# Performance work log

Measured on AMD Instinct MI355X. Metric: run time of the kernel, lower is better.

The kernel has to match this reference:

```python
import jax, jax.numpy as jnp
import numpy as np

N = 16384          # points
DIM = 256          # feature dim
HEADS = 8
HD = DIM // HEADS  # head dim = 32
K = 20             # neighbors
MLP_HID = int(DIM * 4.0)
CHUNK = 2048       # query chunk for kNN (avoids N^2 matrix)
EPS = 1e-5
SCALE = HD ** -0.5


def layernorm(x, w, b):
    m = jnp.mean(x, axis=-1, keepdims=True)
    v = jnp.var(x, axis=-1, keepdims=True)
    return (x - m) * jax.lax.rsqrt(v + EPS) * w + b


def knn_graph(positions):
    """Brute-force kNN (squared L2) computed in query chunks. [N, K] indices, self excluded."""
    def chunk_fn(q):  # q: [CHUNK, 3]
        d = jnp.sum((q[:, None, :] - positions[None, :, :]) ** 2, axis=-1)  # [CHUNK, N]
        _, idx = jax.lax.top_k(-d, K + 1)  # ascending distance; first col is self (dist 0)
        return idx[:, 1:]
    idx = jax.lax.map(chunk_fn, positions.reshape(-1, CHUNK, 3))
    return idx.reshape(-1, K)


def setup_inputs() -> dict:
    key = jax.random.key(0)
    ks = jax.random.split(key, 10)
    w = lambda k, s: jax.random.normal(k, s, jnp.float32) * 0.02
    return {
        "x": jax.random.normal(ks[0], (N, DIM), jnp.float32),
        "positions": jax.random.normal(ks[1], (N, 3), jnp.float32),
        "ln1_w": jnp.ones((DIM,), jnp.float32), "ln1_b": jnp.zeros((DIM,), jnp.float32),
        "Wq": w(ks[2], (DIM, DIM)), "bq": jnp.zeros((DIM,), jnp.float32),
        "Wk": w(ks[3], (DIM, DIM)), "bk": jnp.zeros((DIM,), jnp.float32),
        "Wv": w(ks[4], (DIM, DIM)), "bv": jnp.zeros((DIM,), jnp.float32),
        "Wo": w(ks[5], (DIM, DIM)), "bo": jnp.zeros((DIM,), jnp.float32),
        "ln2_w": jnp.ones((DIM,), jnp.float32), "ln2_b": jnp.zeros((DIM,), jnp.float32),
        "W1": w(ks[6], (MLP_HID, DIM)), "b1": jnp.zeros((MLP_HID,), jnp.float32),
        "W2": w(ks[7], (DIM, MLP_HID)), "b2": jnp.zeros((DIM,), jnp.float32),
    }


def reference(x, positions, ln1_w, ln1_b, Wq, bq, Wk, bk, Wv, bv, Wo, bo,
              ln2_w, ln2_b, W1, b1, W2, b2):
    knn = knn_graph(positions)                      # [N, K] int32
    h = layernorm(x, ln1_w, ln1_b)                  # [N, D]
    q = (h @ Wq.T + bq).reshape(N, HEADS, HD)       # [N, H, hd]
    k = h @ Wk.T + bk                               # [N, D]
    v = h @ Wv.T + bv
    kn = k[knn].reshape(N, K, HEADS, HD)            # gather neighbor keys   [N, K, H, hd]
    vn = v[knn].reshape(N, K, HEADS, HD)            # gather neighbor values
    scores = jnp.einsum('nhd,nkhd->nhk', q, kn) * SCALE  # [N, H, K]
    attn = jax.nn.softmax(scores, axis=-1)
    out = jnp.einsum('nhk,nkhd->nhd', attn, vn).reshape(N, DIM)
    x = x + out @ Wo.T + bo                          # residual 1
    h2 = layernorm(x, ln2_w, ln2_b)
    mlp = jax.nn.gelu(h2 @ W1.T + b1, approximate=False) @ W2.T + b2
    return x + mlp                                   # residual 2
```

## Files before the change

kernel.cpp:

```cpp
#include <hip/hip_runtime.h>
#include <math.h>

#define N_PTS 16384
#define DIMS 256
#define HEADS 8
#define HDIM 32
#define KNN 20
#define MLPH 1024
#define NSHARD 128
#define SHARDC 128
#define SURV_SLOTS 64
#define SCALE 0.17677669529663687f

typedef unsigned short u16;
typedef unsigned long long ull;
typedef __attribute__((ext_vector_type(8))) short bf16x8;
typedef __attribute__((ext_vector_type(8))) unsigned short u16x8;
typedef __attribute__((ext_vector_type(4))) float f32x4;

__device__ __forceinline__ float bf2f(u16 u) {
  return __uint_as_float(((unsigned int)u) << 16);
}
__device__ __forceinline__ u16 f2bf(float f) {
  unsigned int u = __float_as_uint(f);
  u += 0x7fffu + ((u >> 16) & 1u);
  return (u16)(u >> 16);
}
__device__ __forceinline__ float fin(float v) {
  return __builtin_isfinite(v) ? v : 0.f;
}
__device__ __forceinline__ float dist2(float4 a, float4 b) {
  float dx = a.x - b.x, dy = a.y - b.y, dz = a.z - b.z;
  return dx * dx + dy * dy + dz * dz;
}
__device__ __forceinline__ u16x8 cvt8(float4 a, float4 b) {
  u16x8 o;
  o[0] = f2bf(a.x); o[1] = f2bf(a.y); o[2] = f2bf(a.z); o[3] = f2bf(a.w);
  o[4] = f2bf(b.x); o[5] = f2bf(b.y); o[6] = f2bf(b.z); o[7] = f2bf(b.w);
  return o;
}
__device__ __forceinline__ void gld16(const u16* g, u16* l) {
  __builtin_amdgcn_global_load_lds(
      (const __attribute__((address_space(1))) unsigned int*)g,
      (__attribute__((address_space(3))) unsigned int*)l, 16, 0, 0);
}


__global__ __launch_bounds__(256) void knn_init(const float* __restrict__ pos,
                                                float4* __restrict__ pos4,
                                                int* __restrict__ cnt,
                                                int* __restrict__ nbr) {
  int i = blockIdx.x * 256 + threadIdx.x;
  cnt[i] = 0;
#pragma unroll
  for (int j = 0; j < KNN; ++j) nbr[i * KNN + j] = 0;
  float x = fin(pos[3 * i]), y = fin(pos[3 * i + 1]), z = fin(pos[3 * i + 2]);
  pos4[i] = make_float4(x, y, z, x * x + y * y + z * z);
}


__global__ __launch_bounds__(256) void conv_w(const float* __restrict__ Wq,
                                              const float* __restrict__ Wk,
                                              const float* __restrict__ Wv,
                                              const float* __restrict__ Wo,
                                              u16* __restrict__ wbf) {
  int idx = blockIdx.x * 256 + threadIdx.x;
  int mat = idx >> 14, loc = idx & 16383;
  const float* src = (mat == 0) ? Wq : ((mat == 1) ? Wk : ((mat == 2) ? Wv : Wo));
  float4 v = ((const float4*)src)[loc];
  ushort4 o;
  o.x = f2bf(v.x); o.y = f2bf(v.y); o.z = f2bf(v.z); o.w = f2bf(v.w);
  ((ushort4*)(wbf + mat * 65536))[loc] = o;
}


__global__ __launch_bounds__(256) void knn_shardmin(const float4* __restrict__ pos4,
                                                    float* __restrict__ Mmin) {
  __shared__ float4 cp[SHARDC];
  int shard = blockIdx.x;
  int qbase = blockIdx.y * 1024 + threadIdx.x;
  if (threadIdx.x < SHARDC) cp[threadIdx.x] = pos4[shard * SHARDC + threadIdx.x];
  float m2x[4], m2y[4], m2z[4], mn[4];
#pragma unroll
  for (int k = 0; k < 4; ++k) {
    float4 qp = pos4[qbase + k * 256];
    m2x[k] = -2.f * qp.x; m2y[k] = -2.f * qp.y; m2z[k] = -2.f * qp.z;
    mn[k] = 3.4e38f;
  }
  __syncthreads();
#pragma unroll 4
  for (int c = 0; c < SHARDC; ++c) {
    float4 cc = cp[c];
#pragma unroll
    for (int k = 0; k < 4; ++k) {
      float t = fmaf(m2z[k], cc.z, cc.w);
      t = fmaf(m2y[k], cc.y, t);
      t = fmaf(m2x[k], cc.x, t);
      mn[k] = fminf(mn[k], t);
    }
  }
#pragma unroll
  for (int k = 0; k < 4; ++k) Mmin[shard * N_PTS + qbase + k * 256] = mn[k];
}

__global__ __launch_bounds__(256) void knn_tau(const float* __restrict__ Mmin,
                                               float* __restrict__ tau) {
  int q = blockIdx.x * 256 + threadIdx.x;
  float a[21];
#pragma unroll
  for (int j = 0; j < 21; ++j) a[j] = 3.4e38f;
  for (int s = 0; s < NSHARD; ++s) {
    float v = Mmin[s * N_PTS + q];
    a[20] = fminf(a[20], v);
#pragma unroll
    for (int j = 20; j >= 1; --j) {
      float lo = fminf(a[j - 1], a[j]), hi = fmaxf(a[j - 1], a[j]);
      a[j - 1] = lo; a[j] = hi;
    }
  }
  tau[q] = a[20];
}

__global__ __launch_bounds__(256) void knn_collect(const float4* __restrict__ pos4,
                                                   const float* __restrict__ tau,
                                                   int* __restrict__ cnt,
                                                   ull* __restrict__ surv) {
  __shared__ float4 cp[SHARDC];
  int cbase = blockIdx.x * SHARDC;
  int qbase = blockIdx.y * 1024 + threadIdx.x;
  if (threadIdx.x < SHARDC) cp[threadIdx.x] = pos4[cbase + threadIdx.x];
  float4 qp[4];
  float m2x[4], m2y[4], m2z[4], tq[4];
  unsigned int packed[4];
  int hitcnt[4];
#pragma unroll
  for (int k = 0; k < 4; ++k) {
    qp[k] = pos4[qbase + k * 256];
    m2x[k] = -2.f * qp[k].x; m2y[k] = -2.f * qp[k].y; m2z[k] = -2.f * qp[k].z;
    tq[k] = tau[qbase + k * 256] + 2e-4f;
    packed[k] = 0; hitcnt[k] = 0;
  }
  __syncthreads();
#pragma unroll 4
  for (int c = 0; c < SHARDC; ++c) {
    float4 cc = cp[c];
#pragma unroll
    for (int k = 0; k < 4; ++k) {
      float t = fmaf(m2z[k], cc.z, cc.w);
      t = fmaf(m2y[k], cc.y, t);
      t = fmaf(m2x[k], cc.x, t);
      bool hit = (t <= tq[k]);
      packed[k] = hit ? ((packed[k] << 8) | (unsigned)c) : packed[k];
      hitcnt[k] += hit ? 1 : 0;
    }
  }
#pragma unroll
  for (int k = 0; k < 4; ++k) {
    int hc = hitcnt[k];
    if (hc > 0) {
      int q = qbase + k * 256;
      if (hc <= 4) {
        int slot = atomicAdd(&cnt[q], hc);
        for (int i = 0; i < hc; ++i) {
          int c = (packed[k] >> (8 * i)) & 255;
          float d = dist2(qp[k], cp[c]);
          ull key = ((ull)__float_as_uint(d) << 32) | (unsigned)(cbase + c);
          if (slot + i < SURV_SLOTS)
            surv[(size_t)q * SURV_SLOTS + slot + i] = key;
        }
      } else {
        for (int c = 0; c < SHARDC; ++c) {
          float4 cc = cp[c];
          float t = fmaf(m2z[k], cc.z, cc.w);
          t = fmaf(m2y[k], cc.y, t);
          t = fmaf(m2x[k], cc.x, t);
          if (t <= tq[k]) {
            float d = dist2(qp[k], cc);
            ull key = ((ull)__float_as_uint(d) << 32) | (unsigned)(cbase + c);
            int slot = atomicAdd(&cnt[q], 1);
            if (slot < SURV_SLOTS) surv[(size_t)q * SURV_SLOTS + slot] = key;
          }
        }
      }
    }
  }
}

__global__ void knn_rank(const int* __restrict__ cnt,
                         const ull* __restrict__ surv,
                         int* __restrict__ nbr) {
  __shared__ ull s[SURV_SLOTS];
  int q = blockIdx.x;
  int c = min(cnt[q], SURV_SLOTS);
  for (int i = threadIdx.x; i < c; i += 64) s[i] = surv[(size_t)q * SURV_SLOTS + i];
  __syncthreads();
  for (int i = threadIdx.x; i < c; i += 64) {
    ull key = s[i];
    int rank = 0;
    for (int j = 0; j < c; ++j) rank += (s[j] < key);
    if (rank >= 1 && rank <= KNN) nbr[q * KNN + rank - 1] = (int)(key & 0xffffffffu);
  }
}


__global__ __launch_bounds__(256) void ln_kernel(const float* __restrict__ xin,
                                                 const float* __restrict__ w,
                                                 const float* __restrict__ b,
                                                 u16* __restrict__ out) {
  int row = blockIdx.x * 4 + (threadIdx.x >> 6);
  int lane = threadIdx.x & 63;
  float4 u = ((const float4*)(xin + row * DIMS))[lane];
  float f[4] = {fin(u.x), fin(u.y), fin(u.z), fin(u.w)};
  float sum = f[0] + f[1] + f[2] + f[3];
  float sq = f[0] * f[0] + f[1] * f[1] + f[2] * f[2] + f[3] * f[3];
#pragma unroll
  for (int o = 32; o > 0; o >>= 1) {
    sum += __shfl_xor(sum, o);
    sq += __shfl_xor(sq, o);
  }
  float mean = sum * (1.f / 256.f);
  float var = fmaxf(sq * (1.f / 256.f) - mean * mean, 0.f);
  float rs = rsqrtf(var + 1e-5f);
  float4 wv = ((const float4*)w)[lane];
  float4 bv = ((const float4*)b)[lane];
  ushort4 o4;
  o4.x = f2bf(fin((f[0] - mean) * rs * wv.x + bv.x));
  o4.y = f2bf(fin((f[1] - mean) * rs * wv.y + bv.y));
  o4.z = f2bf(fin((f[2] - mean) * rs * wv.z + bv.z));
  o4.w = f2bf(fin((f[3] - mean) * rs * wv.w + bv.w));
  ((ushort4*)(out + row * DIMS))[lane] = o4;
}

template <int EPI, int BW>
__device__ __forceinline__ void gemm_body(const u16* __restrict__ A,
                                          const void* __restrict__ B,
                                          const float* __restrict__ bias,
                                          const float* __restrict__ res,
                                          void* __restrict__ out,
                                          int m0, int n0, int Nc, int K) {
  __shared__ __align__(16) u16 Asm[128 * 32];
  __shared__ __align__(16) u16 Bsm[128 * 32];
  const int t = threadIdx.x;
  const int w = t >> 6, lane = t & 63;
  const int quad = lane >> 4, mr = lane & 15;
  const int wm = (w >> 1) * 64, wn = (w & 1) * 64;
  const int r = t >> 2, sseg = t & 3;

  f32x4 acc[4][4];
  const f32x4 zero4 = {0.f, 0.f, 0.f, 0.f};
#pragma unroll
  for (int i = 0; i < 4; ++i)
#pragma unroll
    for (int j = 0; j < 4; ++j) acc[i][j] = zero4;

  const u16* Ab = A + (size_t)(m0 + r) * K + sseg * 8;
  const u16* Bb16 = (const u16*)B + (size_t)(n0 + r) * K + sseg * 8;
  const float* Bb32 = (const float*)B + (size_t)(n0 + r) * K + sseg * 8;
  u16* AsmT = Asm + t * 8;
  u16* BsmT = Bsm + t * 8;

  for (int k0 = 0; k0 < K; k0 += 32) {
    if (BW) {
      __syncthreads();
      gld16(Ab + k0, AsmT);
      gld16(Ab + k0 + (size_t)64 * K, AsmT + 2048);
      gld16(Bb16 + k0, BsmT);
      gld16(Bb16 + k0 + (size_t)64 * K, BsmT + 2048);
      __syncthreads();
    } else {
      float4 b0a = *(const float4*)(Bb32 + k0);
      float4 b0b = *(const float4*)(Bb32 + k0 + 4);
      float4 b1a = *(const float4*)(Bb32 + k0 + (size_t)64 * K);
      float4 b1b = *(const float4*)(Bb32 + k0 + (size_t)64 * K + 4);
      u16x8 b0 = cvt8(b0a, b0b);
      u16x8 b1 = cvt8(b1a, b1b);
      __syncthreads();
      gld16(Ab + k0, AsmT);
      gld16(Ab + k0 + (size_t)64 * K, AsmT + 2048);
      *(u16x8*)BsmT = b0;
      *(u16x8*)(BsmT + 2048) = b1;
      __syncthreads();
    }
    bf16x8 af[4], bfr[4];
#pragma unroll
    for (int i = 0; i < 4; ++i)
      af[i] = *(const bf16x8*)&Asm[(wm + i * 16 + mr) * 32 + quad * 8];
#pragma unroll
    for (int j = 0; j < 4; ++j)
      bfr[j] = *(const bf16x8*)&Bsm[(wn + j * 16 + mr) * 32 + quad * 8];
#pragma unroll
    for (int i = 0; i < 4; ++i)
#pragma unroll
      for (int j = 0; j < 4; ++j)
        acc[i][j] = __builtin_amdgcn_mfma_f32_16x16x32_bf16(af[i], bfr[j], acc[i][j], 0, 0, 0);
  }

  float* outf = (float*)out;
  u16* outb = (u16*)out;
#pragma unroll
  for (int j = 0; j < 4; ++j) {
    int n = n0 + wn + j * 16 + mr;
    float bv = bias[n];
#pragma unroll
    for (int i = 0; i < 4; ++i) {
      int mb = m0 + wm + i * 16 + quad * 4;
#pragma unroll
      for (int rr = 0; rr < 4; ++rr) {
        size_t off = (size_t)(mb + rr) * Nc + n;
        float v = acc[i][j][rr] + bv;
        if (EPI == 0) {
          outb[off] = f2bf(fin(v));
        } else if (EPI == 1) {
          outf[off] = fin(v + res[off]);
        } else {
          float g = 0.5f * v * (1.0f + erff(v * 0.70710678118654752f));
          outb[off] = f2bf(fin(g));
        }
      }
    }
  }
}

template <int EPI, int BW>
__global__ __launch_bounds__(256) void gemm_bt(const u16* __restrict__ A,
                                               const void* __restrict__ B,
                                               const float* __restrict__ bias,
                                               const float* __restrict__ res,
                                               void* __restrict__ out,
                                               int Nc, int K) {
  gemm_body<EPI, BW>(A, B, bias, res, out, blockIdx.y * 128, blockIdx.x * 128, Nc, K);
}

__global__ __launch_bounds__(256) void gemm_qkv(const u16* __restrict__ A,
                                                const u16* __restrict__ wbf,
                                                const float* __restrict__ bq,
                                                const float* __restrict__ bk,
                                                const float* __restrict__ bv,
                                                u16* __restrict__ qo,
                                                u16* __restrict__ ko,
                                                u16* __restrict__ vo) {
  int sel = blockIdx.x >> 1;
  const u16* B = wbf + sel * 65536;
  const float* bias = (sel == 0) ? bq : ((sel == 1) ? bk : bv);
  u16* out = (sel == 0) ? qo : ((sel == 1) ? ko : vo);
  gemm_body<0, 1>(A, B, bias, nullptr, out, blockIdx.y * 128, (blockIdx.x & 1) * 128,
                  DIMS, DIMS);
}


__global__ __launch_bounds__(256) void attn_kernel(const u16* __restrict__ Q,
                                                   const u16* __restrict__ Kb,
                                                   const u16* __restrict__ Vb,
                                                   const int* __restrict__ nbr,
                                                   u16* __restrict__ out) {
  int t = blockIdx.x * 256 + threadIdx.x;
  int p = t >> 3, h = t & 7;
  const u16* qrow = Q + (size_t)p * DIMS + h * HDIM;
  float qf[32];
#pragma unroll
  for (int c = 0; c < 4; ++c) {
    u16x8 u = *(const u16x8*)(qrow + c * 8);
#pragma unroll
    for (int e = 0; e < 8; ++e) qf[c * 8 + e] = bf2f(u[e]);
  }
  int idx[KNN];
#pragma unroll
  for (int j = 0; j < KNN; ++j) {
    int ix = nbr[p * KNN + j];
    idx[j] = (ix < 0 || ix >= N_PTS) ? 0 : ix;
  }
  float sc[KNN];
#pragma unroll
  for (int j = 0; j < KNN; ++j) {
    const u16* kr = Kb + (size_t)idx[j] * DIMS + h * HDIM;
    float acc = 0.f;
#pragma unroll
    for (int c = 0; c < 4; ++c) {
      u16x8 u = *(const u16x8*)(kr + c * 8);
#pragma unroll
      for (int e = 0; e < 8; ++e) acc += qf[c * 8 + e] * bf2f(u[e]);
    }
    sc[j] = fin(acc * SCALE);
  }
  float mx = sc[0];
#pragma unroll
  for (int j = 1; j < KNN; ++j) mx = fmaxf(mx, sc[j]);
  float sum = 0.f;
#pragma unroll
  for (int j = 0; j < KNN; ++j) {
    sc[j] = expf(sc[j] - mx);
    sum += sc[j];
  }
  float inv = 1.f / fmaxf(sum, 1e-30f);
  float o[32];
#pragma unroll
  for (int d = 0; d < 32; ++d) o[d] = 0.f;
#pragma unroll
  for (int j = 0; j < KNN; ++j) {
    float wgt = sc[j] * inv;
    const u16* vr = Vb + (size_t)idx[j] * DIMS + h * HDIM;
#pragma unroll
    for (int c = 0; c < 4; ++c) {
      u16x8 u = *(const u16x8*)(vr + c * 8);
#pragma unroll
      for (int e = 0; e < 8; ++e) o[c * 8 + e] = fmaf(wgt, bf2f(u[e]), o[c * 8 + e]);
    }
  }
  u16* orow = out + (size_t)p * DIMS + h * HDIM;
#pragma unroll
  for (int c = 0; c < 4; ++c) {
    u16x8 u;
#pragma unroll
    for (int e = 0; e < 8; ++e) u[e] = f2bf(fin(o[c * 8 + e]));
    *(u16x8*)(orow + c * 8) = u;
  }
}

extern "C" void kernel_launch(void* const* d_in, const int* in_sizes, int n_in,
                              void* d_out, int out_size, void* d_ws, size_t ws_size,
                              hipStream_t stream) {
  const float* x = (const float*)d_in[0];
  const float* positions = (const float*)d_in[1];
  const float* ln1_w = (const float*)d_in[2];
  const float* ln1_b = (const float*)d_in[3];
  const float* Wq = (const float*)d_in[4];
  const float* bq = (const float*)d_in[5];
  const float* Wk = (const float*)d_in[6];
  const float* bk = (const float*)d_in[7];
  const float* Wv = (const float*)d_in[8];
  const float* bv = (const float*)d_in[9];
  const float* Wo = (const float*)d_in[10];
  const float* bo = (const float*)d_in[11];
  const float* ln2_w = (const float*)d_in[12];
  const float* ln2_b = (const float*)d_in[13];
  const float* W1 = (const float*)d_in[14];
  const float* b1 = (const float*)d_in[15];
  const float* W2 = (const float*)d_in[16];
  const float* b2 = (const float*)d_in[17];

  char* w = (char*)d_ws;
  const size_t B0 = 16777216;
  float* x1f = (float*)(w + 0);
  u16* hid = (u16*)(w + B0);
  u16* h2 = (u16*)(w + 50331648);
  float4* pos4 = (float4*)(w + B0);
  float* Mmin = (float*)(w + B0 + 262144);
  u16* wbf = (u16*)(w + B0 + 262144);
  float* tau = (float*)(w + B0 + 8650752);
  int* cnt = (int*)(w + B0 + 8716288);
  ull* surv = (ull*)(w + B0 + 8781824);
  int* nbr = (int*)(w + B0 + 25559040);
  u16* h = (u16*)(w + B0 + 26869760);
  u16* qb = (u16*)(w + 0);
  u16* kb = (u16*)(w + 8388608);
  u16* vb = (u16*)(w + B0 + 8781824);
  u16* ao = (u16*)(w + B0 + 17170432);

  knn_init<<<dim3(N_PTS / 256), dim3(256), 0, stream>>>(positions, pos4, cnt, nbr);
  knn_shardmin<<<dim3(NSHARD, 16), dim3(256), 0, stream>>>(pos4, Mmin);
  knn_tau<<<dim3(64), dim3(256), 0, stream>>>(Mmin, tau);
  conv_w<<<dim3(256), dim3(256), 0, stream>>>(Wq, Wk, Wv, Wo, wbf);
  knn_collect<<<dim3(NSHARD, 16), dim3(256), 0, stream>>>(pos4, tau, cnt, surv);
  knn_rank<<<dim3(N_PTS), dim3(64), 0, stream>>>(cnt, surv, nbr);

  ln_kernel<<<dim3(N_PTS / 4), dim3(256), 0, stream>>>(x, ln1_w, ln1_b, h);
  gemm_qkv<<<dim3(6, 128), dim3(256), 0, stream>>>(h, wbf, bq, bk, bv, qb, kb, vb);

  attn_kernel<<<dim3(N_PTS * HEADS / 256), dim3(256), 0, stream>>>(qb, kb, vb, nbr, ao);
  gemm_bt<1, 1><<<dim3(2, 128), dim3(256), 0, stream>>>(ao, wbf + 196608, bo, x, x1f,
                                                        DIMS, DIMS);

  ln_kernel<<<dim3(N_PTS / 4), dim3(256), 0, stream>>>(x1f, ln2_w, ln2_b, h2);
  gemm_bt<2, 0><<<dim3(8, 128), dim3(256), 0, stream>>>(h2, W1, b1, nullptr, hid,
                                                        MLPH, DIMS);
  gemm_bt<1, 0><<<dim3(2, 128), dim3(256), 0, stream>>>(hid, W2, b2, x1f,
                                                        (float*)d_out, DIMS, MLPH);
}
```

Before: 379.6 us.

## Fuse weight conversion into kNN init, pre-convert MLP weights, parallelize tau merge

```diff
diff --git a/kernel.cpp b/kernel.cpp
--- a/kernel.cpp
+++ b/kernel.cpp
@@ -11,6 +11,8 @@
 #define SHARDC 128
 #define SURV_SLOTS 64
 #define SCALE 0.17677669529663687f
+#define WEXT_OFF 58720256
+#define WEXT_BYTES 1572864
 
 typedef unsigned short u16;
 typedef unsigned long long ull;
@@ -43,6 +45,40 @@
   __builtin_amdgcn_global_load_lds(
       (const __attribute__((address_space(1))) unsigned int*)g,
       (__attribute__((address_space(3))) unsigned int*)l, 16, 0, 0);
+}
+
+
+__global__ __launch_bounds__(256) void knn_init_conv(
+    const float* __restrict__ pos, float4* __restrict__ pos4,
+    int* __restrict__ cnt, int* __restrict__ nbr,
+    const float* __restrict__ Wq, const float* __restrict__ Wk,
+    const float* __restrict__ Wv, const float* __restrict__ Wo,
+    const float* __restrict__ W1, const float* __restrict__ W2,
+    u16* __restrict__ ext) {
+  int idx = blockIdx.x * 256 + threadIdx.x;
+  if (idx < N_PTS) {
+    cnt[idx] = 0;
+#pragma unroll
+    for (int j = 0; j < KNN; ++j) nbr[idx * KNN + j] = 0;
+    float x = fin(pos[3 * idx]), y = fin(pos[3 * idx + 1]), z = fin(pos[3 * idx + 2]);
+    pos4[idx] = make_float4(x, y, z, x * x + y * y + z * z);
+  }
+  const float* src;
+  u16* dst;
+  int loc;
+  if (idx < 65536) {
+    int mat = idx >> 14; loc = idx & 16383;
+    src = (mat == 0) ? Wq : ((mat == 1) ? Wk : ((mat == 2) ? Wv : Wo));
+    dst = ext + mat * 65536;
+  } else if (idx < 131072) {
+    loc = idx - 65536; src = W1; dst = ext + 262144;
+  } else {
+    loc = idx - 131072; src = W2; dst = ext + 524288;
+  }
+  float4 v = ((const float4*)src)[loc];
+  ushort4 o;
+  o.x = f2bf(v.x); o.y = f2bf(v.y); o.z = f2bf(v.z); o.w = f2bf(v.w);
+  ((ushort4*)dst)[loc] = o;
 }
 
 
@@ -57,7 +93,6 @@
   float x = fin(pos[3 * i]), y = fin(pos[3 * i + 1]), z = fin(pos[3 * i + 2]);
   pos4[i] = make_float4(x, y, z, x * x + y * y + z * z);
 }
-
 
 __global__ __launch_bounds__(256) void conv_w(const float* __restrict__ Wq,
                                               const float* __restrict__ Wk,
@@ -103,13 +138,17 @@
   for (int k = 0; k < 4; ++k) Mmin[shard * N_PTS + qbase + k * 256] = mn[k];
 }
 
-__global__ __launch_bounds__(256) void knn_tau(const float* __restrict__ Mmin,
-                                               float* __restrict__ tau) {
-  int q = blockIdx.x * 256 + threadIdx.x;
+__global__ __launch_bounds__(256) void knn_tau4(const float* __restrict__ Mmin,
+                                                float* __restrict__ tau) {
+  __shared__ float sm[64][4][21];
+  int tid = threadIdx.x;
+  int sub = tid & 3, qi = tid >> 2;
+  int q = blockIdx.x * 64 + qi;
   float a[21];
 #pragma unroll
   for (int j = 0; j < 21; ++j) a[j] = 3.4e38f;
-  for (int s = 0; s < NSHARD; ++s) {
+  int s0 = sub * 32;
+  for (int s = s0; s < s0 + 32; ++s) {
     float v = Mmin[s * N_PTS + q];
     a[20] = fminf(a[20], v);
 #pragma unroll
@@ -118,7 +157,25 @@
       a[j - 1] = lo; a[j] = hi;
     }
   }
-  tau[q] = a[20];
+#pragma unroll
+  for (int j = 0; j < 21; ++j) sm[qi][sub][j] = a[j];
+  __syncthreads();
+  if (sub == 0) {
+    int i0 = 0, i1 = 0, i2 = 0, i3 = 0;
+    float tv = 3.4e38f;
+#pragma unroll
+    for (int n = 0; n < 21; ++n) {
+      float v0 = sm[qi][0][i0], v1 = sm[qi][1][i1];
+      float v2 = sm[qi][2][i2], v3 = sm[qi][3][i3];
+      float m = fminf(fminf(v0, v1), fminf(v2, v3));
+      tv = m;
+      if (m == v0) ++i0;
+      else if (m == v1) ++i1;
+      else if (m == v2) ++i2;
+      else ++i3;
+    }
+    tau[q] = tv;
+  }
 }
 
 __global__ __launch_bounds__(256) void knn_collect(const float4* __restrict__ pos4,
@@ -445,7 +502,7 @@
   u16* h2 = (u16*)(w + 50331648);
   float4* pos4 = (float4*)(w + B0);
   float* Mmin = (float*)(w + B0 + 262144);
-  u16* wbf = (u16*)(w + B0 + 262144);
+  u16* wbfH = (u16*)(w + B0 + 262144);
   float* tau = (float*)(w + B0 + 8650752);
   int* cnt = (int*)(w + B0 + 8716288);
   ull* surv = (ull*)(w + B0 + 8781824);
@@ -455,24 +512,40 @@
   u16* kb = (u16*)(w + 8388608);
   u16* vb = (u16*)(w + B0 + 8781824);
   u16* ao = (u16*)(w + B0 + 17170432);
-
-  knn_init<<<dim3(N_PTS / 256), dim3(256), 0, stream>>>(positions, pos4, cnt, nbr);
+  u16* wext = (u16*)(w + WEXT_OFF);
+  const bool big = ws_size >= (size_t)WEXT_OFF + WEXT_BYTES;
+
+  if (big) {
+    knn_init_conv<<<dim3(768), dim3(256), 0, stream>>>(
+        positions, pos4, cnt, nbr, Wq, Wk, Wv, Wo, W1, W2, wext);
+  } else {
+    knn_init<<<dim3(N_PTS / 256), dim3(256), 0, stream>>>(positions, pos4, cnt, nbr);
+  }
   knn_shardmin<<<dim3(NSHARD, 16), dim3(256), 0, stream>>>(pos4, Mmin);
-  knn_tau<<<dim3(64), dim3(256), 0, stream>>>(Mmin, tau);
-  conv_w<<<dim3(256), dim3(256), 0, stream>>>(Wq, Wk, Wv, Wo, wbf);
+  knn_tau4<<<dim3(N_PTS / 64), dim3(256), 0, stream>>>(Mmin, tau);
+  if (!big) conv_w<<<dim3(256), dim3(256), 0, stream>>>(Wq, Wk, Wv, Wo, wbfH);
   knn_collect<<<dim3(NSHARD, 16), dim3(256), 0, stream>>>(pos4, tau, cnt, surv);
   knn_rank<<<dim3(N_PTS), dim3(64), 0, stream>>>(cnt, surv, nbr);
 
+  const u16* qkvw = big ? wext : wbfH;
+
   ln_kernel<<<dim3(N_PTS / 4), dim3(256), 0, stream>>>(x, ln1_w, ln1_b, h);
-  gemm_qkv<<<dim3(6, 128), dim3(256), 0, stream>>>(h, wbf, bq, bk, bv, qb, kb, vb);
+  gemm_qkv<<<dim3(6, 128), dim3(256), 0, stream>>>(h, qkvw, bq, bk, bv, qb, kb, vb);
 
   attn_kernel<<<dim3(N_PTS * HEADS / 256), dim3(256), 0, stream>>>(qb, kb, vb, nbr, ao);
-  gemm_bt<1, 1><<<dim3(2, 128), dim3(256), 0, stream>>>(ao, wbf + 196608, bo, x, x1f,
+  gemm_bt<1, 1><<<dim3(2, 128), dim3(256), 0, stream>>>(ao, qkvw + 196608, bo, x, x1f,
                                                         DIMS, DIMS);
 
   ln_kernel<<<dim3(N_PTS / 4), dim3(256), 0, stream>>>(x1f, ln2_w, ln2_b, h2);
-  gemm_bt<2, 0><<<dim3(8, 128), dim3(256), 0, stream>>>(h2, W1, b1, nullptr, hid,
-                                                        MLPH, DIMS);
-  gemm_bt<1, 0><<<dim3(2, 128), dim3(256), 0, stream>>>(hid, W2, b2, x1f,
-                                                        (float*)d_out, DIMS, MLPH);
-}
+  if (big) {
+    gemm_bt<2, 1><<<dim3(8, 128), dim3(256), 0, stream>>>(h2, wext + 262144, b1,
+                                                          nullptr, hid, MLPH, DIMS);
+    gemm_bt<1, 1><<<dim3(2, 128), dim3(256), 0, stream>>>(hid, wext + 524288, b2, x1f,
+                                                          (float*)d_out, DIMS, MLPH);
+  } else {
+    gemm_bt<2, 0><<<dim3(8, 128), dim3(256), 0, stream>>>(h2, W1, b1, nullptr, hid,
+                                                          MLPH, DIMS);
+    gemm_bt<1, 0><<<dim3(2, 128), dim3(256), 0, stream>>>(hid, W2, b2, x1f,
+                                                          (float*)d_out, DIMS, MLPH);
+  }
+}
```

After: 349.9 us (median of 2 runs). -7.8%, faster.
